# Optimization experiments

Measured on AMD Instinct MI355X. Metric: run time of the kernel, lower is better.

The kernel has to match this reference:

```python
import jax, jax.numpy as jnp
import numpy as np

D_MODEL = 1024
HEAD = 16
EPS = 1e-07
B, S = 2, 2048


def _layernorm(x, alpha, bias):
    # torch: (x - mean) / (std + eps), std with Bessel correction (ddof=1)
    mean = jnp.mean(x, axis=-1, keepdims=True)
    std = jnp.std(x, axis=-1, keepdims=True, ddof=1)
    return alpha * ((x - mean) / (std + EPS)) + bias


def setup_inputs() -> dict:
    key = jax.random.key(0)
    ks = jax.random.split(key, 16)
    d = D_MODEL
    sc = 1.0 / np.sqrt(d)
    x = jax.random.normal(ks[0], (B, S, d), dtype=jnp.float32)
    mask = jnp.tril(jnp.ones((S, S), dtype=jnp.float32))[None, None]  # [1,1,S,S] multiplicative causal
    inp = {"x": x, "mask": mask}
    names = ["Wq", "Wk", "Wv", "Wo", "W1", "W2"]
    for i, n in enumerate(names):
        inp[n] = jax.random.normal(ks[1 + i], (d, d), dtype=jnp.float32) * sc
        inp["b" + n[1:].lower()] = jnp.zeros((d,), dtype=jnp.float32)
    inp["alpha1"] = jnp.ones((1,), dtype=jnp.float32)
    inp["beta1"] = jnp.zeros((1,), dtype=jnp.float32)
    inp["alpha2"] = jnp.ones((1,), dtype=jnp.float32)
    inp["beta2"] = jnp.zeros((1,), dtype=jnp.float32)
    return inp


def reference(x, mask, Wq, bq, Wk, bk, Wv, bv, Wo, bo, W1, b1, W2, b2,
              alpha1, beta1, alpha2, beta2):
    b, s, d = x.shape
    h, kd = HEAD, d // HEAD
    # --- residual 1: attention(norm(x)) ---
    y = _layernorm(x, alpha1, beta1)
    q = (y @ Wq.T + bq).reshape(b, s, h, kd).transpose(0, 2, 1, 3)  # [B,H,S,kd]
    k = (y @ Wk.T + bk).reshape(b, s, h, kd).transpose(0, 2, 1, 3)
    v = (y @ Wv.T + bv).reshape(b, s, h, kd).transpose(0, 2, 1, 3)
    scores = jnp.einsum("bhqd,bhkd->bhqk", q, k) / jnp.sqrt(jnp.float32(kd))
    scores = scores * mask  # multiplicative mask (not additive)
    # torch nn.functional.softmax with implicit dim on a 4D tensor -> dim=1 (head axis)
    attn = jax.nn.softmax(scores, axis=1)
    out = jnp.einsum("bhqk,bhkd->bhqd", attn, v)
    out = out.transpose(0, 2, 1, 3).reshape(b, s, d)
    x = x + (out @ Wo.T + bo)  # dropout = identity (eval)
    # --- residual 2: mlp(norm(x)) ---
    y = _layernorm(x, alpha2, beta2)
    hdn = jax.nn.gelu(y @ W1.T + b1, approximate=False)
    x = x + (hdn @ W2.T + b2)
    return x
```

## Files before the change

### kernel.cpp

```cpp
#include <hip/hip_runtime.h>
#include <cstdint>

typedef __bf16 bf16x8 __attribute__((ext_vector_type(8)));
typedef float  f32x4  __attribute__((ext_vector_type(4)));

static constexpr int B_ = 2, S_ = 2048, D_ = 1024, H_ = 16;
static constexpr int NTRI = 136;
static constexpr int QKVS = 3072;

#define DEV static __device__ __forceinline__

DEV ushort f2bf(float f) {
  uint32_t u = __builtin_bit_cast(uint32_t, f);
  u += 0x7fffu + ((u >> 16) & 1u);
  return (ushort)(u >> 16);
}
DEV float bf2f(ushort h) {
  uint32_t u = ((uint32_t)h) << 16;
  return __builtin_bit_cast(float, u);
}
DEV bf16x8 ld16(const ushort* p) {
  return __builtin_bit_cast(bf16x8, *(const int4*)p);
}
DEV f32x4 mfma16(bf16x8 a, bf16x8 b, f32x4 c) {
  return __builtin_amdgcn_mfma_f32_16x16x32_bf16(a, b, c, 0, 0, 0);
}
DEV void gload_lds16(const void* g, void* l) {
  __builtin_amdgcn_global_load_lds(
      (const __attribute__((address_space(1))) char*)g,
      (__attribute__((address_space(3))) char*)l, 16, 0, 0);
}

__global__ __launch_bounds__(256) void k_convw(
    const float* __restrict__ w0, const float* __restrict__ w1,
    const float* __restrict__ w2, const float* __restrict__ w3,
    const float* __restrict__ w4, const float* __restrict__ w5,
    ushort* __restrict__ out) {
  const float* src;
  int z = blockIdx.y;
  switch (z) {
    case 0: src = w0; break; case 1: src = w1; break;
    case 2: src = w2; break; case 3: src = w3; break;
    case 4: src = w4; break; default: src = w5; break;
  }
  size_t i = (size_t)blockIdx.x * 256 + threadIdx.x;
  float4 v = ((const float4*)src)[i];
  ushort4 o;
  o.x = f2bf(v.x); o.y = f2bf(v.y); o.z = f2bf(v.z); o.w = f2bf(v.w);
  ((ushort4*)(out + (size_t)z * 1048576))[i] = o;
}

__global__ __launch_bounds__(256) void k_bcat(const float* __restrict__ bq,
                                              const float* __restrict__ bk,
                                              const float* __restrict__ bv,
                                              float* __restrict__ o) {
  int i = blockIdx.x * 256 + threadIdx.x;
  float v = (i < 1024) ? bq[i] : (i < 2048 ? bk[i - 1024] : bv[i - 2048]);
  o[i] = v;
}

template <int INB>
__global__ __launch_bounds__(256) void k_ln(const void* __restrict__ xv,
                                            const float* __restrict__ alpha,
                                            const float* __restrict__ beta,
                                            ushort* __restrict__ y) {
  int row = blockIdx.x, t = threadIdx.x;
  float4 v;
  if constexpr (INB == 0) {
    v = ((const float4*)((const float*)xv + (size_t)row * D_))[t];
  } else {
    ushort4 u = ((const ushort4*)((const ushort*)xv + (size_t)row * D_))[t];
    v.x = bf2f(u.x); v.y = bf2f(u.y); v.z = bf2f(u.z); v.w = bf2f(u.w);
  }
  float s  = v.x + v.y + v.z + v.w;
  float ss = v.x * v.x + v.y * v.y + v.z * v.z + v.w * v.w;
#pragma unroll
  for (int o = 32; o >= 1; o >>= 1) {
    s  += __shfl_down(s, o, 64);
    ss += __shfl_down(ss, o, 64);
  }
  __shared__ float red[8];
  __shared__ float mv[2];
  int w = t >> 6, lane = t & 63;
  if (lane == 0) { red[w] = s; red[4 + w] = ss; }
  __syncthreads();
  if (t == 0) {
    float st  = red[0] + red[1] + red[2] + red[3];
    float sst = red[4] + red[5] + red[6] + red[7];
    float mean = st * (1.f / D_);
    float var  = (sst - (float)D_ * mean * mean) * (1.f / (D_ - 1));
    mv[0] = mean;
    mv[1] = sqrtf(fmaxf(var, 0.f));
  }
  __syncthreads();
  float mean = mv[0];
  float inv  = alpha[0] / (mv[1] + 1e-7f);
  float b0   = beta[0];
  ushort4 o;
  o.x = f2bf((v.x - mean) * inv + b0);
  o.y = f2bf((v.y - mean) * inv + b0);
  o.z = f2bf((v.z - mean) * inv + b0);
  o.w = f2bf((v.w - mean) * inv + b0);
  ((ushort4*)(y + (size_t)row * D_))[t] = o;
}

template <int MODE>
__global__ __launch_bounds__(256) void k_gemm(const ushort* __restrict__ A,
                                              const ushort* __restrict__ W,
                                              const float* __restrict__ bias,
                                              const void* __restrict__ resid,
                                              void* __restrict__ out,
                                              int M, int N, int K) {
  __shared__ __align__(16) ushort As[128 * 128];
  __shared__ __align__(16) ushort Bs[64 * 128];
  int tid = threadIdx.x, lane = tid & 63, w = tid >> 6;
  int wr = w >> 1, wc = w & 1;
  {
  }
  int L = (int)(blockIdx.y * gridDim.x + blockIdx.x);
  int xcd = L & 7, idx = L >> 3;
  int bxs = xcd * 4 + (idx & 3);
  int bys = idx >> 2;
  int bm = bxs * 128, bn = bys * 64;
  int q15 = lane & 15, kc = lane >> 4;
  f32x4 acc[4][2] = {};
  for (int k0 = 0; k0 < K; k0 += 128) {
#pragma unroll
    for (int r = 0; r < 8; r++) {
      int c = r * 256 + tid;
      int row = c >> 4, seg = c & 15;
      int sseg = seg ^ (row & 15);
      gload_lds16(A + (size_t)(bm + row) * K + k0 + sseg * 8,
                  (char*)As + (r * 256 + w * 64) * 16);
    }
#pragma unroll
    for (int r = 0; r < 4; r++) {
      int c = r * 256 + tid;
      int row = c >> 4, seg = c & 15;
      int sseg = seg ^ (row & 15);
      gload_lds16(W + (size_t)(bn + row) * K + k0 + sseg * 8,
                  (char*)Bs + (r * 256 + w * 64) * 16);
    }
    __syncthreads();
#pragma unroll
    for (int ks = 0; ks < 4; ks++) {
      bf16x8 af[4], bfr[2];
#pragma unroll
      for (int m = 0; m < 4; m++) {
        int row = wr * 64 + m * 16 + q15;
        int sseg = (ks * 4 + kc) ^ (row & 15);
        af[m] = ld16(&As[row * 128 + sseg * 8]);
      }
#pragma unroll
      for (int n = 0; n < 2; n++) {
        int row = wc * 32 + n * 16 + q15;
        int sseg = (ks * 4 + kc) ^ (row & 15);
        bfr[n] = ld16(&Bs[row * 128 + sseg * 8]);
      }
#pragma unroll
      for (int m = 0; m < 4; m++)
#pragma unroll
        for (int n = 0; n < 2; n++)
          acc[m][n] = mfma16(af[m], bfr[n], acc[m][n]);
    }
    __syncthreads();
  }
#pragma unroll
  for (int m = 0; m < 4; m++) {
    int grow0 = bm + wr * 64 + m * 16 + kc * 4;
#pragma unroll
    for (int n = 0; n < 2; n++) {
      int gcol = bn + wc * 32 + n * 16 + q15;
      float bv = bias[gcol];
#pragma unroll
      for (int r = 0; r < 4; r++) {
        size_t idx2 = (size_t)(grow0 + r) * N + gcol;
        float v = acc[m][n][r] + bv;
        if constexpr (MODE == 0) {
          ((ushort*)out)[idx2] = f2bf(v);
        } else if constexpr (MODE == 1) {
          ((ushort*)out)[idx2] = f2bf(v + ((const float*)resid)[idx2]);
        } else if constexpr (MODE == 2) {
          float g = 0.5f * v * (1.f + erff(v * 0.70710678118f));
          ((ushort*)out)[idx2] = f2bf(g);
        } else {
          ((float*)out)[idx2] = v + bf2f(((const ushort*)resid)[idx2]);
        }
      }
    }
  }
}

__global__ __launch_bounds__(256) void k_transpose(const ushort* __restrict__ qkv,
                                                   ushort* __restrict__ vt,
                                                   float* __restrict__ vs) {
  __shared__ ushort t[32][33];
  int b = blockIdx.z;
  int j0 = blockIdx.x * 32, c0 = blockIdx.y * 32;
  int tx = threadIdx.x & 31, ty = threadIdx.x >> 5;
#pragma unroll
  for (int i = 0; i < 4; i++)
    t[ty + i * 8][tx] = qkv[((size_t)b * S_ + j0 + ty + i * 8) * QKVS + 2048 + c0 + tx];
  __syncthreads();
#pragma unroll
  for (int i = 0; i < 4; i++)
    vt[((size_t)b * D_ + c0 + ty + i * 8) * S_ + j0 + tx] = t[tx][ty + i * 8];
  if (ty == 0) {
    float s = 0.f;
#pragma unroll
    for (int j = 0; j < 32; j++) s += bf2f(t[j][tx]);
    atomicAdd(&vs[(size_t)b * D_ + c0 + tx], s);
  }
}

__global__ __launch_bounds__(256) void k_qke(const ushort* __restrict__ qkv,
                                             ushort* __restrict__ wout) {
  int t = blockIdx.x, h = blockIdx.y, b = blockIdx.z;
  int qt = (int)((sqrtf(8.f * t + 1.f) - 1.f) * 0.5f);
  while ((qt + 1) * (qt + 2) / 2 <= t) qt++;
  while (qt * (qt + 1) / 2 > t) qt--;
  int jt = t - qt * (qt + 1) / 2;
  int q0 = qt * 128, j0 = jt * 128;
  int tid = threadIdx.x, lane = tid & 63, w = tid >> 6;
  int q15 = lane & 15, kc = lane >> 4;
  int wq = (w >> 1) * 64, wj = (w & 1) * 64;
  const ushort* qb = qkv + (size_t)b * S_ * QKVS;
  __shared__ __align__(16) ushort T[128 * 128];

  f32x4 acc[4][4] = {};
#pragma unroll
  for (int ks = 0; ks < 2; ks++) {
    bf16x8 af[4], bfr[4];
#pragma unroll
    for (int m = 0; m < 4; m++)
      af[m] = ld16(qb + (size_t)(q0 + wq + m * 16 + q15) * QKVS + h * 64 + ks * 32 + kc * 8);
#pragma unroll
    for (int n = 0; n < 4; n++)
      bfr[n] = ld16(qb + (size_t)(j0 + wj + n * 16 + q15) * QKVS + 1024 + h * 64 + ks * 32 + kc * 8);
#pragma unroll
    for (int m = 0; m < 4; m++)
#pragma unroll
      for (int n = 0; n < 4; n++)
        acc[m][n] = mfma16(af[m], bfr[n], acc[m][n]);
  }
#pragma unroll
  for (int m = 0; m < 4; m++)
#pragma unroll
    for (int n = 0; n < 4; n++)
#pragma unroll
      for (int r = 0; r < 4; r++)
        T[(wq + m * 16 + kc * 4 + r) * 128 + wj + n * 16 + q15] =
            f2bf(__expf(acc[m][n][r] * 0.125f));
  __syncthreads();
  ushort* wt = wout + (((size_t)b * H_ + h) * NTRI + t) * 16384;
#pragma unroll
  for (int rd = 0; rd < 8; rd++) {
    int c = rd * 256 + tid;
    *(int4*)(wt + c * 8) = *(const int4*)(T + c * 8);
  }
}

__global__ __launch_bounds__(256) void k_wnorm(ushort* __restrict__ wpk) {
  int strip = blockIdx.x, t = blockIdx.y, b = blockIdx.z;
  int qt = (int)((sqrtf(8.f * t + 1.f) - 1.f) * 0.5f);
  while ((qt + 1) * (qt + 2) / 2 <= t) qt++;
  while (qt * (qt + 1) / 2 > t) qt--;
  int jt = t - qt * (qt + 1) / 2;
  int cell = strip * 2048 + threadIdx.x * 8;
  int row = cell >> 7, col = cell & 127;
  int q = qt * 128 + row;
  int j0 = jt * 128 + col;
  const size_t HSTR = (size_t)NTRI * 16384;
  size_t base = ((size_t)b * H_) * HSTR + (size_t)t * 16384 + cell;

  int4 ch[16];
#pragma unroll
  for (int h = 0; h < 16; h++) ch[h] = *(const int4*)(wpk + base + h * HSTR);
  float s[8] = {};
#pragma unroll
  for (int h = 0; h < 16; h++) {
    const ushort* u = (const ushort*)&ch[h];
#pragma unroll
    for (int i = 0; i < 8; i++) s[i] += bf2f(u[i]);
  }
  float inv[8];
#pragma unroll
  for (int i = 0; i < 8; i++) inv[i] = 1.f / s[i];
#pragma unroll
  for (int h = 0; h < 16; h++) {
    const ushort* u = (const ushort*)&ch[h];
    ushort o[8];
#pragma unroll
    for (int i = 0; i < 8; i++) {
      float wv = bf2f(u[i]) * inv[i] - 0.0625f;
      o[i] = (j0 + i <= q) ? f2bf(wv) : (ushort)0;
    }
    *(int4*)(wpk + base + h * HSTR) = *(int4*)o;
  }
}

__global__ __launch_bounds__(256) void k_pv4(const ushort* __restrict__ wpk,
                                             const ushort* __restrict__ vt,
                                             const float* __restrict__ vsum,
                                             ushort* __restrict__ og) {
  __shared__ __align__(16) ushort As[128 * 128];
  __shared__ __align__(16) ushort Bs[64 * 128];
  int qt = 15 - (int)blockIdx.x, h = blockIdx.y, b = blockIdx.z;
  const ushort* wbh = wpk + ((size_t)b * H_ + h) * NTRI * 16384 +
                      (size_t)(qt * (qt + 1) / 2) * 16384;
  const ushort* vtb = vt + ((size_t)b * D_ + h * 64) * S_;
  int tid = threadIdx.x, lane = tid & 63, w = tid >> 6;
  int q15 = lane & 15, kc = lane >> 4;
  int wr = w >> 1, wc = w & 1;
  f32x4 acc[4][2] = {};
  int nsteps = qt + 1;
  for (int s = 0; s < nsteps; s++) {
    const ushort* wtile = wbh + (size_t)s * 16384;
    int j0 = s * 128;
#pragma unroll
    for (int r = 0; r < 8; r++) {
      int c = r * 256 + tid;
      int row = c >> 4, seg = c & 15;
      int sseg = seg ^ (row & 15);
      gload_lds16(wtile + row * 128 + sseg * 8,
                  (char*)As + (r * 256 + w * 64) * 16);
    }
#pragma unroll
    for (int r = 0; r < 4; r++) {
      int c = r * 256 + tid;
      int row = c >> 4, seg = c & 15;
      int sseg = seg ^ (row & 15);
      gload_lds16(vtb + (size_t)row * S_ + j0 + sseg * 8,
                  (char*)Bs + (r * 256 + w * 64) * 16);
    }
    __syncthreads();
#pragma unroll
    for (int ks = 0; ks < 4; ks++) {
      bf16x8 af[4], bfv[2];
#pragma unroll
      for (int m = 0; m < 4; m++) {
        int row = wr * 64 + m * 16 + q15;
        int sseg = (ks * 4 + kc) ^ (row & 15);
        af[m] = ld16(&As[row * 128 + sseg * 8]);
      }
#pragma unroll
      for (int n = 0; n < 2; n++) {
        int row = wc * 32 + n * 16 + q15;
        int sseg = (ks * 4 + kc) ^ (row & 15);
        bfv[n] = ld16(&Bs[row * 128 + sseg * 8]);
      }
#pragma unroll
      for (int m = 0; m < 4; m++)
#pragma unroll
        for (int n = 0; n < 2; n++)
          acc[m][n] = mfma16(af[m], bfv[n], acc[m][n]);
    }
    __syncthreads();
  }
#pragma unroll
  for (int m = 0; m < 4; m++) {
    int grow0 = qt * 128 + wr * 64 + m * 16 + kc * 4;
#pragma unroll
    for (int n = 0; n < 2; n++) {
      int gcol = h * 64 + wc * 32 + n * 16 + q15;
      float vsv = vsum[b * D_ + gcol] * 0.0625f;
#pragma unroll
      for (int r = 0; r < 4; r++)
        og[((size_t)b * S_ + grow0 + r) * D_ + gcol] = f2bf(acc[m][n][r] + vsv);
    }
  }
}

extern "C" void kernel_launch(void* const* d_in, const int* in_sizes, int n_in,
                              void* d_out, int out_size, void* d_ws, size_t ws_size,
                              hipStream_t stream) {
  const float* x  = (const float*)d_in[0];
  const float* Wq = (const float*)d_in[2];  const float* bq = (const float*)d_in[3];
  const float* Wk = (const float*)d_in[4];  const float* bk = (const float*)d_in[5];
  const float* Wv = (const float*)d_in[6];  const float* bv = (const float*)d_in[7];
  const float* Wo = (const float*)d_in[8];  const float* bo = (const float*)d_in[9];
  const float* W1 = (const float*)d_in[10]; const float* b1 = (const float*)d_in[11];
  const float* W2 = (const float*)d_in[12]; const float* b2 = (const float*)d_in[13];
  const float* a1 = (const float*)d_in[14]; const float* be1 = (const float*)d_in[15];
  const float* a2 = (const float*)d_in[16]; const float* be2 = (const float*)d_in[17];

  char* ws = (char*)d_ws;
  const size_t MB = 1024ull * 1024ull;
  ushort* wb   = (ushort*)(ws);
  ushort* yb   = (ushort*)(ws + 12 * MB);
  ushort* qkvb = (ushort*)(ws + 20 * MB);
  ushort* vtb  = (ushort*)(ws + 44 * MB);
  ushort* x2b  = (ushort*)(ws + 52 * MB);
  ushort* hb   = (ushort*)(ws + 68 * MB);
  float*  vs   = (float*)(ws + 76 * MB);
  float*  bcat = (float*)(ws + 76 * MB + 65536);
  ushort* wpk  = (ushort*)(ws + 80 * MB);

  ushort* wqkv = wb;
  ushort* wob = wb + 3 * 1048576;
  ushort* w1b = wb + 4 * 1048576;
  ushort* w2b = wb + 5 * 1048576;

  const int M = B_ * S_, N = D_, K = D_;

  hipMemsetAsync(vs, 0, (size_t)B_ * D_ * sizeof(float), stream);
  k_convw<<<dim3(1024, 6), 256, 0, stream>>>(Wq, Wk, Wv, Wo, W1, W2, wb);
  k_bcat<<<12, 256, 0, stream>>>(bq, bk, bv, bcat);
  k_ln<0><<<M, 256, 0, stream>>>(x, a1, be1, yb);
  k_gemm<0><<<dim3(32, 48), 256, 0, stream>>>(yb, wqkv, bcat, nullptr, qkvb, M, QKVS, K);
  k_transpose<<<dim3(64, 32, 2), 256, 0, stream>>>(qkvb, vtb, vs);
  k_qke<<<dim3(NTRI, 16, 2), 256, 0, stream>>>(qkvb, wpk);
  k_wnorm<<<dim3(8, NTRI, 2), 256, 0, stream>>>(wpk);
  k_pv4<<<dim3(16, 16, 2), 256, 0, stream>>>(wpk, vtb, vs, yb);
  k_gemm<1><<<dim3(32, 16), 256, 0, stream>>>(yb, wob, bo, x, x2b, M, N, K);
  k_ln<1><<<M, 256, 0, stream>>>(x2b, a2, be2, yb);
  k_gemm<2><<<dim3(32, 16), 256, 0, stream>>>(yb, w1b, b1, nullptr, hb, M, N, K);
  k_gemm<3><<<dim3(32, 16), 256, 0, stream>>>(hb, w2b, b2, x2b, (float*)d_out, M, N, K);
}
```

Before: 251.7 us.

## Fuse QK exp and cross-head softmax normalization into one kernel

Merges the QK^T exponent kernel and the head-axis normalization kernel into one. Each 1024-thread block handles all 16 heads for a 32-row slice of one triangular tile, so the per-position sum over heads is computed in shared memory. This removes a full write and re-read of the unnormalized exp weights to global memory, plus one launch. In exchange each block uses about 150KB of shared memory and 1024 threads, which limits occupancy to one block per CU. Normalization now uses the fp32 exp values rather than values rounded to bf16 first.

Result: faster. 242.2 us (median of 2 runs) (-3.8%).

```diff
diff --git a/kernel.cpp b/kernel.cpp
--- a/kernel.cpp
+++ b/kernel.cpp
@@ -115,8 +115,6 @@
   __shared__ __align__(16) ushort Bs[64 * 128];
   int tid = threadIdx.x, lane = tid & 63, w = tid >> 6;
   int wr = w >> 1, wc = w & 1;
-  {
-  }
   int L = (int)(blockIdx.y * gridDim.x + blockIdx.x);
   int xcd = L & 7, idx = L >> 3;
   int bxs = xcd * 4 + (idx & 3);
@@ -213,89 +211,78 @@
   }
 }
 
-__global__ __launch_bounds__(256) void k_qke(const ushort* __restrict__ qkv,
-                                             ushort* __restrict__ wout) {
-  int t = blockIdx.x, h = blockIdx.y, b = blockIdx.z;
+__global__ __launch_bounds__(1024) void k_qkwn(const ushort* __restrict__ qkv,
+                                               ushort* __restrict__ wout) {
+  int qs = blockIdx.x, t = blockIdx.y, b = blockIdx.z;
   int qt = (int)((sqrtf(8.f * t + 1.f) - 1.f) * 0.5f);
   while ((qt + 1) * (qt + 2) / 2 <= t) qt++;
   while (qt * (qt + 1) / 2 > t) qt--;
   int jt = t - qt * (qt + 1) / 2;
-  int q0 = qt * 128, j0 = jt * 128;
-  int tid = threadIdx.x, lane = tid & 63, w = tid >> 6;
+  int q0 = qt * 128 + qs * 32;
+  int j0 = jt * 128;
+  int tid = threadIdx.x;
+  int h = tid >> 6, lane = tid & 63;
   int q15 = lane & 15, kc = lane >> 4;
-  int wq = (w >> 1) * 64, wj = (w & 1) * 64;
   const ushort* qb = qkv + (size_t)b * S_ * QKVS;
-  __shared__ __align__(16) ushort T[128 * 128];
-
-  f32x4 acc[4][4] = {};
+
+  __shared__ __align__(16) ushort El[16][32][132];
+  __shared__ __align__(16) float invL[32][132];
+
+  f32x4 acc[2][8] = {};
 #pragma unroll
   for (int ks = 0; ks < 2; ks++) {
-    bf16x8 af[4], bfr[4];
-#pragma unroll
-    for (int m = 0; m < 4; m++)
-      af[m] = ld16(qb + (size_t)(q0 + wq + m * 16 + q15) * QKVS + h * 64 + ks * 32 + kc * 8);
-#pragma unroll
-    for (int n = 0; n < 4; n++)
-      bfr[n] = ld16(qb + (size_t)(j0 + wj + n * 16 + q15) * QKVS + 1024 + h * 64 + ks * 32 + kc * 8);
-#pragma unroll
-    for (int m = 0; m < 4; m++)
-#pragma unroll
-      for (int n = 0; n < 4; n++)
-        acc[m][n] = mfma16(af[m], bfr[n], acc[m][n]);
-  }
-#pragma unroll
-  for (int m = 0; m < 4; m++)
-#pragma unroll
-    for (int n = 0; n < 4; n++)
-#pragma unroll
-      for (int r = 0; r < 4; r++)
-        T[(wq + m * 16 + kc * 4 + r) * 128 + wj + n * 16 + q15] =
-            f2bf(__expf(acc[m][n][r] * 0.125f));
+    bf16x8 qf0 = ld16(qb + (size_t)(q0 + q15) * QKVS + h * 64 + ks * 32 + kc * 8);
+    bf16x8 qf1 = ld16(qb + (size_t)(q0 + 16 + q15) * QKVS + h * 64 + ks * 32 + kc * 8);
+#pragma unroll
+    for (int nt = 0; nt < 8; nt++) {
+      bf16x8 kf = ld16(qb + (size_t)(j0 + nt * 16 + q15) * QKVS + 1024 + h * 64 + ks * 32 + kc * 8);
+      acc[0][nt] = mfma16(qf0, kf, acc[0][nt]);
+      acc[1][nt] = mfma16(qf1, kf, acc[1][nt]);
+    }
+  }
+#pragma unroll
+  for (int mt = 0; mt < 2; mt++)
+#pragma unroll
+    for (int nt = 0; nt < 8; nt++)
+#pragma unroll
+      for (int r = 0; r < 4; r++) {
+        float e = __expf(acc[mt][nt][r] * 0.125f);
+        acc[mt][nt][r] = e;
+        El[h][mt * 16 + kc * 4 + r][nt * 16 + q15] = f2bf(e);
+      }
   __syncthreads();
-  ushort* wt = wout + (((size_t)b * H_ + h) * NTRI + t) * 16384;
-#pragma unroll
-  for (int rd = 0; rd < 8; rd++) {
-    int c = rd * 256 + tid;
-    *(int4*)(wt + c * 8) = *(const int4*)(T + c * 8);
-  }
-}
-
-__global__ __launch_bounds__(256) void k_wnorm(ushort* __restrict__ wpk) {
-  int strip = blockIdx.x, t = blockIdx.y, b = blockIdx.z;
-  int qt = (int)((sqrtf(8.f * t + 1.f) - 1.f) * 0.5f);
-  while ((qt + 1) * (qt + 2) / 2 <= t) qt++;
-  while (qt * (qt + 1) / 2 > t) qt--;
-  int jt = t - qt * (qt + 1) / 2;
-  int cell = strip * 2048 + threadIdx.x * 8;
-  int row = cell >> 7, col = cell & 127;
-  int q = qt * 128 + row;
-  int j0 = jt * 128 + col;
-  const size_t HSTR = (size_t)NTRI * 16384;
-  size_t base = ((size_t)b * H_) * HSTR + (size_t)t * 16384 + cell;
-
-  int4 ch[16];
-#pragma unroll
-  for (int h = 0; h < 16; h++) ch[h] = *(const int4*)(wpk + base + h * HSTR);
-  float s[8] = {};
-#pragma unroll
-  for (int h = 0; h < 16; h++) {
-    const ushort* u = (const ushort*)&ch[h];
-#pragma unroll
-    for (int i = 0; i < 8; i++) s[i] += bf2f(u[i]);
-  }
-  float inv[8];
-#pragma unroll
-  for (int i = 0; i < 8; i++) inv[i] = 1.f / s[i];
-#pragma unroll
-  for (int h = 0; h < 16; h++) {
-    const ushort* u = (const ushort*)&ch[h];
-    ushort o[8];
-#pragma unroll
-    for (int i = 0; i < 8; i++) {
-      float wv = bf2f(u[i]) * inv[i] - 0.0625f;
-      o[i] = (j0 + i <= q) ? f2bf(wv) : (ushort)0;
-    }
-    *(int4*)(wpk + base + h * HSTR) = *(int4*)o;
+  {
+    int c = tid * 4;
+    int row = c >> 7, col = c & 127;
+    float s0 = 0.f, s1 = 0.f, s2 = 0.f, s3 = 0.f;
+#pragma unroll
+    for (int hh = 0; hh < 16; hh++) {
+      ushort4 e4 = *(const ushort4*)&El[hh][row][col];
+      s0 += bf2f(e4.x); s1 += bf2f(e4.y); s2 += bf2f(e4.z); s3 += bf2f(e4.w);
+    }
+    float4 iv;
+    iv.x = 1.f / s0; iv.y = 1.f / s1; iv.z = 1.f / s2; iv.w = 1.f / s3;
+    *(float4*)&invL[row][col] = iv;
+  }
+  __syncthreads();
+#pragma unroll
+  for (int mt = 0; mt < 2; mt++)
+#pragma unroll
+    for (int nt = 0; nt < 8; nt++)
+#pragma unroll
+      for (int r = 0; r < 4; r++) {
+        int row = mt * 16 + kc * 4 + r;
+        int col = nt * 16 + q15;
+        float wv = acc[mt][nt][r] * invL[row][col] - 0.0625f;
+        wv = (q0 + row >= j0 + col) ? wv : 0.f;
+        El[h][row][col] = f2bf(wv);
+      }
+  ushort* wt = wout + (((size_t)b * H_ + h) * NTRI + t) * 16384 + (size_t)qs * 32 * 128;
+#pragma unroll
+  for (int it = 0; it < 8; it++) {
+    int row = it * 4 + (lane >> 4);
+    int chunk = lane & 15;
+    *(int4*)(wt + row * 128 + chunk * 8) = *(const int4*)&El[h][row][chunk * 8];
   }
 }
 
@@ -409,8 +396,7 @@
   k_ln<0><<<M, 256, 0, stream>>>(x, a1, be1, yb);
   k_gemm<0><<<dim3(32, 48), 256, 0, stream>>>(yb, wqkv, bcat, nullptr, qkvb, M, QKVS, K);
   k_transpose<<<dim3(64, 32, 2), 256, 0, stream>>>(qkvb, vtb, vs);
-  k_qke<<<dim3(NTRI, 16, 2), 256, 0, stream>>>(qkvb, wpk);
-  k_wnorm<<<dim3(8, NTRI, 2), 256, 0, stream>>>(wpk);
+  k_qkwn<<<dim3(4, NTRI, 2), 1024, 0, stream>>>(qkvb, wpk);
   k_pv4<<<dim3(16, 16, 2), 256, 0, stream>>>(wpk, vtb, vs, yb);
   k_gemm<1><<<dim3(32, 16), 256, 0, stream>>>(yb, wob, bo, x, x2b, M, N, K);
   k_ln<1><<<M, 256, 0, stream>>>(x2b, a2, be2, yb);
```
